# Kernel tuning notes

Measured on AMD Instinct MI355X. Metric: run time of the kernel, lower is better.

The kernel has to match this reference:

```python
import jax, jax.numpy as jnp
import numpy as np

DIM = 384
K = 7          # kernel_size
FINAL = 16     # final_size
DROP_P = 0.2


def setup_inputs() -> dict:
    key = jax.random.key(0)
    k1, k2, k3, k4, k5, k6 = jax.random.split(key, 6)
    hr_feats = jax.random.normal(k1, (8, DIM, 112, 112), jnp.float32)
    guidance = jnp.zeros((1,), jnp.float32)  # unused by forward
    dropout_u = jax.random.uniform(k2, (8, FINAL, FINAL, 1), jnp.float32)
    aw = jax.random.normal(k3, (DIM,), jnp.float32) / np.sqrt(DIM).astype(np.float32)
    ab = 0.01 * jax.random.normal(k4, (1,), jnp.float32)
    w = 1.0 + 0.01 * jax.random.normal(k5, (K, K), jnp.float32)
    b = 0.01 * jax.random.normal(k6, (K, K), jnp.float32)
    return {"hr_feats": hr_feats, "guidance": guidance, "dropout_u": dropout_u,
            "aw": aw, "ab": ab, "w": w, "b": b}


def _unfold_patches(x):
    # x: [b, c, h, w] -> [b, nH, nW, K*K, c], matching torch Unfold + reshape/permute
    bs, c, h, wd = x.shape
    stride = (h - K) // (FINAL - 1)
    nH = FINAL
    nW = FINAL * (wd // h)
    r = (jnp.arange(nH) * stride)[:, None] + jnp.arange(K)      # [nH, K]
    cc = (jnp.arange(nW) * stride)[:, None] + jnp.arange(K)     # [nW, K]
    # advanced indexing -> [b, c, nH, nW, K, K]
    patches = x[:, :, r[:, None, :, None], cc[None, :, None, :]]
    # (kh, kw) flattened row-major, channel last -> same ordering as torch Unfold
    return patches.transpose(0, 2, 3, 4, 5, 1).reshape(bs, nH, nW, K * K, c)


def reference(hr_feats, guidance, dropout_u, aw, ab, w, b):
    patches = _unfold_patches(hr_feats)                    # [b, H, W, P, C]
    # attention_net (eval-mode Dropout is identity): Linear(dim, 1)
    logits = jnp.einsum('bhwpc,c->bhwp', patches, aw) + ab[0]
    mask = (dropout_u > DROP_P).astype(logits.dtype)       # [b, H, W, 1]
    attn_logits = logits * mask * w.reshape(1, 1, 1, -1) + b.reshape(1, 1, 1, -1)
    attn = jax.nn.softmax(attn_logits, axis=-1)            # softmax over patches
    return jnp.einsum('bhwpc,bhwp->bchw', patches, attn)   # [b, C, H, W]
```

## Files before the change

kernel.cpp:

```cpp
#include <hip/hip_runtime.h>
#include <cmath>

#define DIM 384
#define IMG 112
#define IMG2 (IMG*IMG)
#define FINALN 16
#define PATCH 49
#define DROP_P 0.2f

__global__ __launch_bounds__(512, 4) void kFused(const float* __restrict__ hr,
                                                 const float* __restrict__ du,
                                                 const float* __restrict__ aw,
                                                 const float* __restrict__ ab,
                                                 const float* __restrict__ wmat,
                                                 const float* __restrict__ bmat,
                                                 float* __restrict__ out) {
    __shared__ float sp[DIM * PATCH];
    __shared__ float s_aw[DIM];
    __shared__ float s_red[8 * PATCH];

    int tid = threadIdx.x;

    int id  = blockIdx.x;
    int nid = (id & 7) * 256 + (id >> 3);
    int b = nid >> 8;
    int h = (nid >> 4) & 15;
    int w = nid & 15;

    float duv = 0.f, abv = 0.f, wv = 0.f, bv = 0.f;
    if (tid < 64) {
        if (tid < PATCH) { wv = wmat[tid]; bv = bmat[tid]; }
        duv = du[(b << 8) + (h << 4) + w];
        abv = ab[0];
    }
    for (int i = tid; i < DIM; i += 512) s_aw[i] = aw[i];

    const float* base = hr + (size_t)b * DIM * IMG2 + (size_t)(7 * h) * IMG + 7 * w;
    {
        int g = tid >> 3;
        int j = tid & 7;
        const float* gp = base + (size_t)g * 6 * IMG2 + j;
        float* lp = sp + g * 6 * PATCH + j;
        if (j < 7) {
            float v[42];
            #pragma unroll
            for (int it = 0; it < 42; ++it) {
                const int cc = it / 7, s = it % 7;
                v[it] = gp[(size_t)cc * IMG2 + s * IMG];
            }
            #pragma unroll
            for (int it = 0; it < 42; ++it) {
                const int cc = it / 7, s = it % 7;
                lp[cc * PATCH + s * 7] = v[it];
            }
        }
    }
    __syncthreads();

    if (tid < 8 * PATCH) {
        int g = tid / PATCH;
        int p = tid - g * PATCH;
        int c0 = g * 48;
        float acc = 0.f;
        #pragma unroll 8
        for (int c = 0; c < 48; ++c)
            acc = fmaf(sp[(c0 + c) * PATCH + p], s_aw[c0 + c], acc);
        s_red[tid] = acc;
    }
    __syncthreads();

    if (tid < 64) {
        float al = -1e30f;
        if (tid < PATCH) {
            float logit = abv;
            #pragma unroll
            for (int g = 0; g < 8; ++g) logit += s_red[g * PATCH + tid];
            float mask = (duv > DROP_P) ? 1.0f : 0.0f;
            al = fmaf(logit * mask, wv, bv);
        }
        float m = al;
        #pragma unroll
        for (int d = 32; d >= 1; d >>= 1) m = fmaxf(m, __shfl_xor(m, d, 64));
        float e = (tid < PATCH) ? __expf(al - m) : 0.f;
        float s = e;
        #pragma unroll
        for (int d = 32; d >= 1; d >>= 1) s += __shfl_xor(s, d, 64);
        if (tid < PATCH) s_red[tid] = e / s;
    }
    __syncthreads();

    if (tid < DIM) {
        const float* pc = sp + tid * PATCH;
        float acc = 0.f;
        #pragma unroll
        for (int p = 0; p < PATCH; ++p)
            acc = fmaf(pc[p], s_red[p], acc);
        out[(((size_t)b * DIM + tid) * FINALN + h) * FINALN + w] = acc;
    }
}

extern "C" void kernel_launch(void* const* d_in, const int* in_sizes, int n_in,
                              void* d_out, int out_size, void* d_ws, size_t ws_size,
                              hipStream_t stream) {
    const float* hr   = (const float*)d_in[0];
    const float* du   = (const float*)d_in[2];
    const float* aw   = (const float*)d_in[3];
    const float* ab   = (const float*)d_in[4];
    const float* wmat = (const float*)d_in[5];
    const float* bmat = (const float*)d_in[6];
    float* out = (float*)d_out;

    kFused<<<2048, 512, 0, stream>>>(hr, du, aw, ab, wmat, bmat, out);
}
```

Measured before the change: 243.4 us.

## Fuse logit dot-product into patch load with wave shuffle reduction

Each thread now computes partial attention logits from its register-held patch values during the global load, reduces them across lanes with xor shuffles, and writes per-wave partials to shared memory. This removes a separate shared-memory pass and one barrier, and drops the shared aw buffer. The patch tile stride is padded to 50 so the final weighted sum can read float2 pairs from shared memory. It adds shuffle work and register pressure under the 512x4 launch bound.

```diff
diff --git a/kernel.cpp b/kernel.cpp
--- a/kernel.cpp
+++ b/kernel.cpp
@@ -6,6 +6,7 @@
 #define IMG2 (IMG*IMG)
 #define FINALN 16
 #define PATCH 49
+#define SPST 50
 #define DROP_P 0.2f
 
 __global__ __launch_bounds__(512, 4) void kFused(const float* __restrict__ hr,
@@ -15,8 +16,7 @@
                                                  const float* __restrict__ wmat,
                                                  const float* __restrict__ bmat,
                                                  float* __restrict__ out) {
-    __shared__ float sp[DIM * PATCH];
-    __shared__ float s_aw[DIM];
+    __shared__ float sp[DIM * SPST];
     __shared__ float s_red[8 * PATCH];
 
     int tid = threadIdx.x;
@@ -33,39 +33,44 @@
         duv = du[(b << 8) + (h << 4) + w];
         abv = ab[0];
     }
-    for (int i = tid; i < DIM; i += 512) s_aw[i] = aw[i];
 
+    int g = tid >> 3;
+    int j = tid & 7;
     const float* base = hr + (size_t)b * DIM * IMG2 + (size_t)(7 * h) * IMG + 7 * w;
-    {
-        int g = tid >> 3;
-        int j = tid & 7;
-        const float* gp = base + (size_t)g * 6 * IMG2 + j;
-        float* lp = sp + g * 6 * PATCH + j;
-        if (j < 7) {
-            float v[42];
-            #pragma unroll
-            for (int it = 0; it < 42; ++it) {
-                const int cc = it / 7, s = it % 7;
-                v[it] = gp[(size_t)cc * IMG2 + s * IMG];
-            }
-            #pragma unroll
-            for (int it = 0; it < 42; ++it) {
-                const int cc = it / 7, s = it % 7;
-                lp[cc * PATCH + s * 7] = v[it];
-            }
+    const float* gp = base + (size_t)g * 6 * IMG2 + j;
+
+    float awr[6];
+    #pragma unroll
+    for (int cc = 0; cc < 6; ++cc) awr[cc] = aw[g * 6 + cc];
+
+    float part[7] = {0.f, 0.f, 0.f, 0.f, 0.f, 0.f, 0.f};
+    if (j < 7) {
+        float v[42];
+        #pragma unroll
+        for (int it = 0; it < 42; ++it) {
+            const int cc = it / 7, s = it % 7;
+            v[it] = gp[(size_t)cc * IMG2 + s * IMG];
+        }
+        float* lp = sp + g * 6 * SPST + j;
+        #pragma unroll
+        for (int it = 0; it < 42; ++it) {
+            const int cc = it / 7, s = it % 7;
+            lp[cc * SPST + s * 7] = v[it];
+            part[s] = fmaf(v[it], awr[cc], part[s]);
         }
     }
-    __syncthreads();
 
-    if (tid < 8 * PATCH) {
-        int g = tid / PATCH;
-        int p = tid - g * PATCH;
-        int c0 = g * 48;
-        float acc = 0.f;
-        #pragma unroll 8
-        for (int c = 0; c < 48; ++c)
-            acc = fmaf(sp[(c0 + c) * PATCH + p], s_aw[c0 + c], acc);
-        s_red[tid] = acc;
+    #pragma unroll
+    for (int s = 0; s < 7; ++s) {
+        part[s] += __shfl_xor(part[s], 8, 64);
+        part[s] += __shfl_xor(part[s], 16, 64);
+        part[s] += __shfl_xor(part[s], 32, 64);
+    }
+    int wave = tid >> 6, lane = tid & 63;
+    if (lane < 7) {
+        #pragma unroll
+        for (int s = 0; s < 7; ++s)
+            s_red[wave * PATCH + s * 7 + lane] = part[s];
     }
     __syncthreads();
 
@@ -74,7 +79,7 @@
         if (tid < PATCH) {
             float logit = abv;
             #pragma unroll
-            for (int g = 0; g < 8; ++g) logit += s_red[g * PATCH + tid];
+            for (int gg = 0; gg < 8; ++gg) logit += s_red[gg * PATCH + tid];
             float mask = (duv > DROP_P) ? 1.0f : 0.0f;
             al = fmaf(logit * mask, wv, bv);
         }
@@ -90,11 +95,15 @@
     __syncthreads();
 
     if (tid < DIM) {
-        const float* pc = sp + tid * PATCH;
+        const float* pc = sp + tid * SPST;
         float acc = 0.f;
         #pragma unroll
-        for (int p = 0; p < PATCH; ++p)
-            acc = fmaf(pc[p], s_red[p], acc);
+        for (int k = 0; k < 24; ++k) {
+            float2 v2 = *reinterpret_cast<const float2*>(pc + 2 * k);
+            acc = fmaf(v2.x, s_red[2 * k],     acc);
+            acc = fmaf(v2.y, s_red[2 * k + 1], acc);
+        }
+        acc = fmaf(pc[48], s_red[48], acc);
         out[(((size_t)b * DIM + tid) * FINALN + h) * FINALN + w] = acc;
     }
 }
```

After: 244.8 us. About the same (+0.6%).
